# Kernel tuning notes

Measured on AMD Instinct MI355X. Metric: run time of the kernel, lower is better.

Reference implementation:

```python
import jax, jax.numpy as jnp
import numpy as np

BN_EPS = 1e-5


def grid_sample_bilinear(img, grid):
    """Torch F.grid_sample, mode=bilinear, padding_mode=zeros, align_corners=False.
    img: (B, C, H, W); grid: (B, N, 2) in [-1, 1] -> (B, C, N)."""
    B, C, H, W = img.shape
    x = ((grid[..., 0] + 1.0) * W - 1.0) * 0.5  # (B, N) pixel coords
    y = ((grid[..., 1] + 1.0) * H - 1.0) * 0.5
    x0 = jnp.floor(x)
    y0 = jnp.floor(y)
    x1 = x0 + 1.0
    y1 = y0 + 1.0
    wx1 = x - x0
    wx0 = 1.0 - wx1
    wy1 = y - y0
    wy0 = 1.0 - wy1
    img_flat = img.reshape(B, C, H * W)

    def corner(xi, yi, w):
        valid = (xi >= 0) & (xi <= W - 1) & (yi >= 0) & (yi <= H - 1)
        xi_c = jnp.clip(xi, 0, W - 1).astype(jnp.int32)
        yi_c = jnp.clip(yi, 0, H - 1).astype(jnp.int32)
        idx = yi_c * W + xi_c  # (B, N)
        vals = jnp.take_along_axis(img_flat, idx[:, None, :], axis=2)  # (B, C, N)
        return vals * (w * valid.astype(img.dtype))[:, None, :]

    return (corner(x0, y0, wx0 * wy0) + corner(x1, y0, wx1 * wy0)
            + corner(x0, y1, wx0 * wy1) + corner(x1, y1, wx1 * wy1))


def conv1x1(x, w, b):
    # x: (B, Cin, N), w: (Cout, Cin), b: (Cout,)
    return jnp.einsum('oi,bin->bon', w, x) + b[None, :, None]


def batchnorm1d_train(x, gamma, beta):
    # training-mode BN over (batch, length) per channel, biased variance
    mean = jnp.mean(x, axis=(0, 2), keepdims=True)
    var = jnp.mean((x - mean) ** 2, axis=(0, 2), keepdims=True)
    xn = (x - mean) * jax.lax.rsqrt(var + BN_EPS)
    return xn * gamma[None, :, None] + beta[None, :, None]


def setup_inputs() -> dict:
    key = jax.random.key(0)
    ks = jax.random.split(key, 12)
    B, N, CI, CP, H, W, R = 4, 16384, 256, 256, 64, 160, 4
    Cin = CI + CP
    Cb = CP // R

    def glorot(k, shape):
        fan_in = shape[1]
        return jax.random.normal(k, shape, dtype=jnp.float32) * (1.0 / np.sqrt(fan_in))

    return {
        'pts_img': jax.random.uniform(ks[0], (B, N, 2), dtype=jnp.float32, minval=-1.0, maxval=1.0),
        'img_feats': jax.random.normal(ks[1], (B, CI, H, W), dtype=jnp.float32),
        'pts_feats': jax.random.normal(ks[2], (B, CP, N), dtype=jnp.float32),
        'fusion_w': glorot(ks[3], (CP, Cin)),
        'fusion_b': jax.random.normal(ks[4], (CP,), dtype=jnp.float32) * 0.01,
        'bn_gamma': jnp.ones((CP,), dtype=jnp.float32),
        'bn_beta': jnp.zeros((CP,), dtype=jnp.float32),
        'ca1_w': glorot(ks[5], (Cb, CP)),
        'ca1_b': jax.random.normal(ks[6], (Cb,), dtype=jnp.float32) * 0.01,
        'ca2_w': glorot(ks[7], (CP, Cb)),
        'ca2_b': jax.random.normal(ks[8], (CP,), dtype=jnp.float32) * 0.01,
        'sa_w': glorot(ks[9], (Cb, CP)),
        'sa_b': jax.random.normal(ks[10], (Cb,), dtype=jnp.float32) * 0.01,
    }


def reference(pts_img, img_feats, pts_feats, fusion_w, fusion_b, bn_gamma, bn_beta,
              ca1_w, ca1_b, ca2_w, ca2_b, sa_w, sa_b):
    # grid_sample gather: (B, C_I, N)
    pts_wise_img_feats = grid_sample_bilinear(img_feats, pts_img)
    fusion = jnp.concatenate([pts_wise_img_feats, pts_feats], axis=1)  # (B, C_I+C_P, N)
    # fusion MLP: conv1x1 + BN + ReLU
    fusion = jax.nn.relu(batchnorm1d_train(conv1x1(fusion, fusion_w, fusion_b), bn_gamma, bn_beta))
    # spatial attention: max over channels of bottleneck conv, sigmoid gate
    spatial = jax.nn.sigmoid(jnp.max(conv1x1(fusion, sa_w, sa_b), axis=1, keepdims=True))
    fusion = spatial * fusion
    # channel attention: bottleneck MLP, global max-pool over points, sigmoid gate
    ca = conv1x1(jax.nn.relu(conv1x1(fusion, ca1_w, ca1_b)), ca2_w, ca2_b)  # (B, C_P, N)
    channel = jax.nn.sigmoid(jnp.max(ca, axis=2, keepdims=True))  # (B, C_P, 1)
    return channel * fusion
```

## Files before the change

kernel.cpp:

```cpp
#include <hip/hip_runtime.h>
#include <stdint.h>


typedef __attribute__((ext_vector_type(8))) short bf16x8;
typedef __attribute__((ext_vector_type(4))) float f32x4;

#define B_ 4
#define N_ 16384
#define H_ 64
#define W_ 160
#define HW_ (H_ * W_)
#define K_ 512

__device__ __forceinline__ float bf2f(unsigned short u) {
    union { unsigned int i; float f; } c; c.i = ((unsigned int)u) << 16; return c.f;
}
__device__ __forceinline__ unsigned short f2bf(float f) {
    union { float f; unsigned int i; } c; c.f = f;
    unsigned int u = c.i;
    return (unsigned short)((u + 0x7FFFu + ((u >> 16) & 1u)) >> 16);
}
__device__ __forceinline__ unsigned int fkey(float f) {
    union { float f; unsigned int u; int i; } c; c.f = f;
    return (c.i < 0) ? ~c.u : (c.u | 0x80000000u);
}
__device__ __forceinline__ float funkey(unsigned int k) {
    union { unsigned int u; float f; } c;
    c.u = (k & 0x80000000u) ? (k & 0x7FFFFFFFu) : ~k;
    return c.f;
}

__device__ __forceinline__ void async_copy16(void* lds, const void* g) {
#if defined(__has_builtin) && __has_builtin(__builtin_amdgcn_global_load_lds)
    __builtin_amdgcn_global_load_lds(
        (const __attribute__((address_space(1))) unsigned int*)g,
        (__attribute__((address_space(3))) unsigned int*)lds, 16, 0, 0);
#else
    *(uint4*)lds = *(const uint4*)g;
#endif
}

__global__ __launch_bounds__(256) void k_imgt(const float* __restrict__ img,
                                              unsigned short* __restrict__ imgT,
                                              const float* __restrict__ fw,
                                              const float* __restrict__ saw,
                                              const float* __restrict__ c1w,
                                              const float* __restrict__ c2w,
                                              unsigned short* WfB, unsigned short* saB,
                                              unsigned short* ca1B, unsigned short* ca2B,
                                              float* buckets, unsigned int* camax) {
    int t = threadIdx.x;
    int bx = blockIdx.x;
    if (bx < 2560) {
        __shared__ __align__(16) unsigned short tile[64 * 68];
        int hw0 = (bx % 160) * 64, c0 = ((bx / 160) & 3) * 64, b = bx / 640;
        const float* src = img + ((size_t)b * 256 + c0) * HW_ + hw0;
        int sub = (t & 15) * 4, grp = t >> 4;
#pragma unroll
        for (int it = 0; it < 4; ++it) {
            int cl = grp + it * 16;
            float4 v = *(const float4*)(src + (size_t)cl * HW_ + sub);
            ushort4 o;
            o.x = f2bf(v.x); o.y = f2bf(v.y); o.z = f2bf(v.z); o.w = f2bf(v.w);
            *(ushort4*)(tile + cl * 68 + sub) = o;
        }
        __syncthreads();
        unsigned short* dst = imgT + ((size_t)b * HW_ + hw0) * 256 + c0;
#pragma unroll
        for (int it = 0; it < 4; ++it) {
            int hwl = grp + it * 16;
            ushort4 o;
            o.x = tile[(sub + 0) * 68 + hwl];
            o.y = tile[(sub + 1) * 68 + hwl];
            o.z = tile[(sub + 2) * 68 + hwl];
            o.w = tile[(sub + 3) * 68 + hwl];
            *(ushort4*)(dst + (size_t)hwl * 256 + sub) = o;
        }
    } else {
        int j = bx - 2560;
        if (j == 0) {
            for (int i = t; i < 16 * 512; i += 256) buckets[i] = 0.f;
            for (int i = t; i < 8 * 1024; i += 256) camax[i] = 0u;
        }
        int i = j * 256 + t;
        if (i < 131072) WfB[i] = f2bf(fw[i]);
        else if (i < 147456) saB[i - 131072] = f2bf(saw[i - 131072]);
        else if (i < 163840) ca1B[i - 147456] = f2bf(c1w[i - 147456]);
        else if (i < 180224) ca2B[i - 163840] = f2bf(c2w[i - 163840]);
    }
}

__global__ __launch_bounds__(256, 4) void k_gemm1f(const unsigned short* __restrict__ WfB,
                                                   const float* __restrict__ pim,
                                                   const unsigned short* __restrict__ imgT,
                                                   const float* __restrict__ pts,
                                                   const float* __restrict__ fb,
                                                   unsigned short* __restrict__ Y,
                                                   float* __restrict__ buckets) {
    __shared__ __align__(16) char smem[38912];
    unsigned short* At = (unsigned short*)smem;
    unsigned short* Bt = (unsigned short*)(smem + 16384);
    unsigned short* tile = (unsigned short*)smem;
    uint4*  offs4 = (uint4*)(smem + 33792);
    float4* wts4  = (float4*)(smem + 34816);
    float* biasS = (float*)(smem + 35840);
    float* redS  = (float*)(smem + 36864);
    float* redQ  = (float*)(smem + 37888);

    int t = threadIdx.x;
    int n0 = blockIdx.x * 64, bb = blockIdx.y;
    int w = t >> 6, lane = t & 63, quad = lane >> 4, l15 = lane & 15;
    const unsigned short* imb = imgT + (size_t)bb * HW_ * 256;

    if (t < 64) {
        float2 g2 = *(const float2*)(pim + (size_t)((size_t)bb * N_ + n0 + t) * 2);
        float x = (g2.x + 1.0f) * (0.5f * W_) - 0.5f;
        float y = (g2.y + 1.0f) * (0.5f * H_) - 0.5f;
        float xf = floorf(x), yf = floorf(y);
        float wx1 = x - xf, wx0 = 1.0f - wx1;
        float wy1 = y - yf, wy0 = 1.0f - wy1;
        int x0 = (int)xf, y0 = (int)yf;
        int x1 = x0 + 1, y1 = y0 + 1;
        float vx0 = (x0 >= 0 && x0 < W_) ? 1.f : 0.f;
        float vx1 = (x1 >= 0 && x1 < W_) ? 1.f : 0.f;
        float vy0 = (y0 >= 0 && y0 < H_) ? 1.f : 0.f;
        float vy1 = (y1 >= 0 && y1 < H_) ? 1.f : 0.f;
        int cx0 = min(max(x0, 0), W_ - 1), cx1 = min(max(x1, 0), W_ - 1);
        int cy0 = min(max(y0, 0), H_ - 1), cy1 = min(max(y1, 0), H_ - 1);
        uint4 o4;
        o4.x = (unsigned)(cy0 * W_ + cx0);
        o4.y = (unsigned)(cy0 * W_ + cx1);
        o4.z = (unsigned)(cy1 * W_ + cx0);
        o4.w = (unsigned)(cy1 * W_ + cx1);
        offs4[t] = o4;
        float4 w4;
        w4.x = wx0 * wy0 * vx0 * vy0;
        w4.y = wx1 * wy0 * vx1 * vy0;
        w4.z = wx0 * wy1 * vx0 * vy1;
        w4.w = wx1 * wy1 * vx1 * vy1;
        wts4[t] = w4;
    }
    biasS[t] = fb[t];

    const f32x4 fzero = {0.f, 0.f, 0.f, 0.f};
    f32x4 acc[4][4];
#pragma unroll
    for (int i = 0; i < 4; ++i)
#pragma unroll
        for (int j = 0; j < 4; ++j) acc[i][j] = fzero;

    for (int kt = 0; kt < 16; ++kt) {
        int k0 = kt * 32;
        __syncthreads();
#pragma unroll
        for (int q = 0; q < 4; ++q) {
            int row = q * 64 + (t >> 2);
            async_copy16(At + (size_t)q * 2048 + (size_t)t * 8,
                         WfB + (size_t)row * K_ + k0 + (t & 3) * 8);
        }
        if (kt < 8) {
            int pt = t >> 2, cg = t & 3;
            uint4 o4 = offs4[pt];
            float4 w4 = wts4[pt];
            int ch = k0 + cg * 8;
            uint4 cA = *(const uint4*)(imb + (size_t)o4.x * 256 + ch);
            uint4 cB = *(const uint4*)(imb + (size_t)o4.y * 256 + ch);
            uint4 cC = *(const uint4*)(imb + (size_t)o4.z * 256 + ch);
            uint4 cD = *(const uint4*)(imb + (size_t)o4.w * 256 + ch);
            const unsigned short* pa = (const unsigned short*)&cA;
            const unsigned short* pb = (const unsigned short*)&cB;
            const unsigned short* pc = (const unsigned short*)&cC;
            const unsigned short* pd = (const unsigned short*)&cD;
            uint4 ov;
            unsigned short* po = (unsigned short*)&ov;
#pragma unroll
            for (int e = 0; e < 8; ++e)
                po[e] = f2bf(w4.x * bf2f(pa[e]) + w4.y * bf2f(pb[e]) +
                             w4.z * bf2f(pc[e]) + w4.w * bf2f(pd[e]));
            *(uint4*)(Bt + pt * 40 + cg * 8) = ov;
        } else {
            int c_local = t & 31, g = t >> 5;
            int c = (kt - 8) * 32 + c_local;
            const float* src = pts + ((size_t)bb * 256 + c) * (size_t)N_ + n0 + g * 8;
            float4 v0 = *(const float4*)(src + 0);
            float4 v1 = *(const float4*)(src + 4);
            unsigned short* dst = Bt + (size_t)(g * 8) * 40 + c_local;
            dst[0 * 40] = f2bf(v0.x); dst[1 * 40] = f2bf(v0.y);
            dst[2 * 40] = f2bf(v0.z); dst[3 * 40] = f2bf(v0.w);
            dst[4 * 40] = f2bf(v1.x); dst[5 * 40] = f2bf(v1.y);
            dst[6 * 40] = f2bf(v1.z); dst[7 * 40] = f2bf(v1.w);
        }
        __syncthreads();
        bf16x8 af[4], bv[4];
#pragma unroll
        for (int j = 0; j < 4; ++j)
            bv[j] = *(const bf16x8*)(Bt + (j * 16 + l15) * 40 + quad * 8);
#pragma unroll
        for (int i = 0; i < 4; ++i)
            af[i] = *(const bf16x8*)(At + (w * 64 + i * 16 + l15) * 32 + quad * 8);
#pragma unroll
        for (int i = 0; i < 4; ++i)
#pragma unroll
            for (int j = 0; j < 4; ++j)
                acc[i][j] = __builtin_amdgcn_mfma_f32_16x16x32_bf16(af[i], bv[j], acc[i][j], 0, 0, 0);
    }

    __syncthreads();
#pragma unroll
    for (int i = 0; i < 4; ++i) {
        int mloc = w * 64 + i * 16 + quad * 4;
        float b0 = biasS[mloc + 0], b1 = biasS[mloc + 1];
        float b2 = biasS[mloc + 2], b3 = biasS[mloc + 3];
        float s0 = 0.f, q0 = 0.f, s1 = 0.f, q1 = 0.f;
        float s2 = 0.f, q2 = 0.f, s3 = 0.f, q3 = 0.f;
#pragma unroll
        for (int j = 0; j < 4; ++j) {
            int n = j * 16 + l15;
            float y0 = acc[i][j][0] + b0;
            float y1 = acc[i][j][1] + b1;
            float y2 = acc[i][j][2] + b2;
            float y3 = acc[i][j][3] + b3;
            s0 += y0; q0 += y0 * y0;
            s1 += y1; q1 += y1 * y1;
            s2 += y2; q2 += y2 * y2;
            s3 += y3; q3 += y3 * y3;
            ushort4 o;
            o.x = f2bf(y0); o.y = f2bf(y1); o.z = f2bf(y2); o.w = f2bf(y3);
            *(ushort4*)(tile + n * 264 + mloc) = o;
        }
#pragma unroll
        for (int d = 1; d < 16; d <<= 1) {
            s0 += __shfl_xor(s0, d, 64); q0 += __shfl_xor(q0, d, 64);
            s1 += __shfl_xor(s1, d, 64); q1 += __shfl_xor(q1, d, 64);
            s2 += __shfl_xor(s2, d, 64); q2 += __shfl_xor(q2, d, 64);
            s3 += __shfl_xor(s3, d, 64); q3 += __shfl_xor(q3, d, 64);
        }
        if (l15 == 0) {
            redS[mloc + 0] = s0; redQ[mloc + 0] = q0;
            redS[mloc + 1] = s1; redQ[mloc + 1] = q1;
            redS[mloc + 2] = s2; redQ[mloc + 2] = q2;
            redS[mloc + 3] = s3; redQ[mloc + 3] = q3;
        }
    }
    __syncthreads();
    {
        float* bk = buckets + (size_t)(blockIdx.x & 15) * 512;
        atomicAdd(bk + t, redS[t]);
        atomicAdd(bk + 256 + t, redQ[t]);
    }
    size_t Yrow0 = ((size_t)bb * N_ + n0) * 256;
#pragma unroll
    for (int pass = 0; pass < 8; ++pass) {
        int row = pass * 8 + (t >> 5);
        int col = (t & 31) * 8;
        *(uint4*)(Y + Yrow0 + (size_t)row * 256 + col) = *(const uint4*)(tile + row * 264 + col);
    }
}

__global__ __launch_bounds__(256, 2) void k_gate(const unsigned short* __restrict__ Y,
                                                 const float* __restrict__ buckets,
                                                 const float* __restrict__ gamma,
                                                 const float* __restrict__ beta,
                                                 const unsigned short* __restrict__ saB,
                                                 const float* __restrict__ sab,
                                                 const unsigned short* __restrict__ c1B,
                                                 const float* __restrict__ c1b,
                                                 const unsigned short* __restrict__ c2B,
                                                 unsigned int* __restrict__ camax,
                                                 float* __restrict__ sp_g,
                                                 float* __restrict__ ss_out) {
    __shared__ __align__(16) unsigned short Ft[64 * 264];
    __shared__ __align__(16) unsigned short Ht[64 * 72];
    __shared__ float scS[256], shS[256];
    __shared__ float saPart[4][64];
    __shared__ float spL[64];
    int t = threadIdx.x;
    size_t pts0 = (size_t)blockIdx.x * 64;
    int b = (int)(pts0 >> 14);
    int w = t >> 6, lane = t & 63, quad = lane >> 4, l15 = lane & 15;
    int jrow = w * 16 + l15;

    bf16x8 bvs[8], bvc[8];
#pragma unroll
    for (int kt = 0; kt < 8; ++kt) {
        bvs[kt] = *(const bf16x8*)(saB + (size_t)jrow * 256 + kt * 32 + quad * 8);
        bvc[kt] = *(const bf16x8*)(c1B + (size_t)jrow * 256 + kt * 32 + quad * 8);
    }
    float sbias = sab[jrow];
    float cbias = c1b[jrow];

    {
        float s = 0.f, q = 0.f;
#pragma unroll
        for (int bk = 0; bk < 16; ++bk) {
            s += buckets[bk * 512 + t];
            q += buckets[bk * 512 + 256 + t];
        }
        const float inv = 1.0f / (float)(B_ * N_);
        float mean = s * inv;
        float var = q * inv - mean * mean;
        float sc = gamma[t] * rsqrtf(var + 1e-5f);
        float sh = beta[t] - mean * sc;
        scS[t] = sc;
        shS[t] = sh;
        if (blockIdx.x == 0) { ss_out[t] = sc; ss_out[256 + t] = sh; }
    }
    __syncthreads();

    int cc = (t * 8) & 255;
    float scr[8], shr[8];
#pragma unroll
    for (int e = 0; e < 8; ++e) { scr[e] = scS[cc + e]; shr[e] = shS[cc + e]; }
    for (int idx = t * 8; idx < 64 * 256; idx += 2048) {
        int r = idx >> 8;
        uint4 v = *(const uint4*)(Y + (pts0 + r) * 256 + cc);
        unsigned short* us = (unsigned short*)&v;
#pragma unroll
        for (int e = 0; e < 8; ++e) {
            float f = bf2f(us[e]) * scr[e] + shr[e];
            us[e] = f2bf(fmaxf(f, 0.f));
        }
        *(uint4*)(Ft + r * 264 + cc) = v;
    }
    __syncthreads();

    const f32x4 fzero = {0.f, 0.f, 0.f, 0.f};
    f32x4 accS[4], accC[4];
#pragma unroll
    for (int i = 0; i < 4; ++i) { accS[i] = fzero; accC[i] = fzero; }
#pragma unroll
    for (int kt = 0; kt < 8; ++kt) {
        bf16x8 af[4];
#pragma unroll
        for (int i = 0; i < 4; ++i)
            af[i] = *(const bf16x8*)(Ft + (i * 16 + l15) * 264 + kt * 32 + quad * 8);
#pragma unroll
        for (int i = 0; i < 4; ++i) {
            accS[i] = __builtin_amdgcn_mfma_f32_16x16x32_bf16(af[i], bvs[kt], accS[i], 0, 0, 0);
            accC[i] = __builtin_amdgcn_mfma_f32_16x16x32_bf16(af[i], bvc[kt], accC[i], 0, 0, 0);
        }
    }
#pragma unroll
    for (int i = 0; i < 4; ++i) {
#pragma unroll
        for (int r = 0; r < 4; ++r) {
            float v = accS[i][r] + sbias;
#pragma unroll
            for (int d = 1; d < 16; d <<= 1) v = fmaxf(v, __shfl_xor(v, d, 64));
            if (l15 == 0) saPart[w][i * 16 + quad * 4 + r] = v;
        }
    }
    __syncthreads();
    if (t < 64) {
        float m4 = fmaxf(fmaxf(saPart[0][t], saPart[1][t]),
                         fmaxf(saPart[2][t], saPart[3][t]));
        float sv = 1.0f / (1.0f + __expf(-m4));
        spL[t] = sv;
        sp_g[pts0 + t] = sv;
    }
    __syncthreads();

#pragma unroll
    for (int i = 0; i < 4; ++i) {
#pragma unroll
        for (int r = 0; r < 4; ++r) {
            int pt = i * 16 + quad * 4 + r;
            float hv = fmaxf(accC[i][r] * spL[pt] + cbias, 0.f);
            Ht[pt * 72 + jrow] = f2bf(hv);
        }
    }
    __syncthreads();

    {
        bf16x8 b2a[4], b2b[4];
#pragma unroll
        for (int mt = 0; mt < 4; ++mt) {
            b2a[mt] = *(const bf16x8*)(c2B + (size_t)(w * 64 + mt * 16 + l15) * 64 + quad * 8);
            b2b[mt] = *(const bf16x8*)(c2B + (size_t)(w * 64 + mt * 16 + l15) * 64 + 32 + quad * 8);
        }
        float vmax[4] = {-3e38f, -3e38f, -3e38f, -3e38f};
#pragma unroll
        for (int i = 0; i < 4; ++i) {
            bf16x8 a0 = *(const bf16x8*)(Ht + (i * 16 + l15) * 72 + quad * 8);
            bf16x8 a1 = *(const bf16x8*)(Ht + (i * 16 + l15) * 72 + 32 + quad * 8);
#pragma unroll
            for (int mt = 0; mt < 4; ++mt) {
                f32x4 acc = __builtin_amdgcn_mfma_f32_16x16x32_bf16(a0, b2a[mt], fzero, 0, 0, 0);
                acc = __builtin_amdgcn_mfma_f32_16x16x32_bf16(a1, b2b[mt], acc, 0, 0, 0);
#pragma unroll
                for (int r = 0; r < 4; ++r) vmax[mt] = fmaxf(vmax[mt], acc[r]);
            }
        }
        unsigned int* cam = camax + (size_t)(blockIdx.x & 7) * 1024 + b * 256;
#pragma unroll
        for (int mt = 0; mt < 4; ++mt) {
            float v = vmax[mt];
            v = fmaxf(v, __shfl_xor(v, 16, 64));
            v = fmaxf(v, __shfl_xor(v, 32, 64));
            if (quad == 0) atomicMax(cam + w * 64 + mt * 16 + l15, fkey(v));
        }
    }
}

__global__ __launch_bounds__(256) void k_out(const unsigned short* __restrict__ Y,
                                             const unsigned int* __restrict__ camax,
                                             const float* __restrict__ c2b,
                                             const float* __restrict__ ss,
                                             const float* __restrict__ sp_g,
                                             float* __restrict__ out) {
    __shared__ __align__(16) unsigned short tile[64 * 68];
    __shared__ float ch[64], scT[64], shT[64], spT[64];
    int t = threadIdx.x;
    int n0 = blockIdx.x * 64, m0 = blockIdx.y * 64, b = blockIdx.z;
    if (t < 64) {
        int m = m0 + t;
        unsigned int k = 0u;
#pragma unroll
        for (int bk = 0; bk < 8; ++bk) k = max(k, camax[bk * 1024 + b * 256 + m]);
        ch[t] = 1.0f / (1.0f + __expf(-(funkey(k) + c2b[m])));
        scT[t] = ss[m];
        shT[t] = ss[256 + m];
        spT[t] = sp_g[(size_t)b * N_ + n0 + t];
    }
    int sub = (t & 15) * 4, grp = t >> 4;
    const unsigned short* src = Y + ((size_t)b * N_ + n0) * 256 + m0;
#pragma unroll
    for (int it = 0; it < 4; ++it) {
        int nl = grp + it * 16;
        ushort4 v = *(const ushort4*)(src + (size_t)nl * 256 + sub);
        *(ushort4*)(tile + nl * 68 + sub) = v;
    }
    __syncthreads();
    float* dst = out + ((size_t)b * 256 + m0) * N_ + n0;
#pragma unroll
    for (int it = 0; it < 4; ++it) {
        int ml = grp + it * 16;
        float g = ch[ml], scv = scT[ml], shv = shT[ml];
        float4 o;
        o.x = fmaxf(bf2f(tile[(sub + 0) * 68 + ml]) * scv + shv, 0.f) * spT[sub + 0] * g;
        o.y = fmaxf(bf2f(tile[(sub + 1) * 68 + ml]) * scv + shv, 0.f) * spT[sub + 1] * g;
        o.z = fmaxf(bf2f(tile[(sub + 2) * 68 + ml]) * scv + shv, 0.f) * spT[sub + 2] * g;
        o.w = fmaxf(bf2f(tile[(sub + 3) * 68 + ml]) * scv + shv, 0.f) * spT[sub + 3] * g;
        *(float4*)(dst + (size_t)ml * N_ + sub) = o;
    }
}

extern "C" void kernel_launch(void* const* d_in, const int* in_sizes, int n_in,
                              void* d_out, int out_size, void* d_ws, size_t ws_size,
                              hipStream_t stream) {
    (void)in_sizes; (void)n_in; (void)out_size; (void)ws_size;
    const float* pts_img = (const float*)d_in[0];
    const float* img     = (const float*)d_in[1];
    const float* pts     = (const float*)d_in[2];
    const float* fw      = (const float*)d_in[3];
    const float* fbias   = (const float*)d_in[4];
    const float* gamma   = (const float*)d_in[5];
    const float* beta    = (const float*)d_in[6];
    const float* c1w     = (const float*)d_in[7];
    const float* c1b     = (const float*)d_in[8];
    const float* c2w     = (const float*)d_in[9];
    const float* c2b     = (const float*)d_in[10];
    const float* saw     = (const float*)d_in[11];
    const float* sab     = (const float*)d_in[12];
    float* out = (float*)d_out;

    char* ws = (char*)d_ws;
    unsigned short* imgT = (unsigned short*)(ws);
    unsigned short* Y    = (unsigned short*)(ws + 20971520);
    unsigned short* WfB  = (unsigned short*)(ws + 54525952);
    unsigned short* saB  = (unsigned short*)(ws + 54788096);
    unsigned short* ca1B = (unsigned short*)(ws + 54820864);
    unsigned short* ca2B = (unsigned short*)(ws + 54853632);
    float* buckets       = (float*)(ws + 54886400);
    unsigned int* camax  = (unsigned int*)(ws + 54919168);
    float* sp_g          = (float*)(ws + 54951936);
    float* ss            = (float*)(ws + 55214080);

    k_imgt<<<3264, 256, 0, stream>>>(img, imgT, fw, saw, c1w, c2w,
                                     WfB, saB, ca1B, ca2B, buckets, camax);
    k_gemm1f<<<dim3(256, 4), 256, 0, stream>>>(WfB, pts_img, imgT, pts, fbias, Y, buckets);
    k_gate<<<1024, 256, 0, stream>>>(Y, buckets, gamma, beta, saB, sab, ca1B, c1b,
                                     ca2B, camax, sp_g, ss);
    k_out<<<dim3(256, 4, 4), 256, 0, stream>>>(Y, camax, c2b, ss, sp_g, out);
}
```

Before: 248.4 us.

## Software-prefetch next K-tile gather and point features into registers

The global loads for the bilinear image gather and the point-feature tile of step kt+1 are now issued right after the barrier, before the MFMA work of step kt. The tile is converted and stored to shared memory at the start of the next iteration, so global latency is meant to hide behind compute instead of sitting between the two barriers. Sample offsets and weights are read from shared memory once, after an added barrier. This raises register pressure (four uint4 plus two float4 stay live across the MFMA loop), which may reduce occupancy.

```diff
diff --git a/kernel.cpp b/kernel.cpp
--- a/kernel.cpp
+++ b/kernel.cpp
@@ -141,6 +141,25 @@
         wts4[t] = w4;
     }
     biasS[t] = fb[t];
+    __syncthreads();
+
+    int pt = t >> 2, cg = t & 3;
+    float4 w4 = wts4[pt];
+    uint4 o4r = offs4[pt];
+    const unsigned short* pA = imb + (size_t)o4r.x * 256 + cg * 8;
+    const unsigned short* pB = imb + (size_t)o4r.y * 256 + cg * 8;
+    const unsigned short* pC = imb + (size_t)o4r.z * 256 + cg * 8;
+    const unsigned short* pD = imb + (size_t)o4r.w * 256 + cg * 8;
+    int c_local = t & 31, g = t >> 5;
+    const float* psrc = pts + ((size_t)bb * 256 + c_local) * (size_t)N_ + n0 + g * 8;
+
+    uint4 gA, gB, gC, gD;
+    float4 p0, p1;
+
+    gA = *(const uint4*)(pA);
+    gB = *(const uint4*)(pB);
+    gC = *(const uint4*)(pC);
+    gD = *(const uint4*)(pD);
 
     const f32x4 fzero = {0.f, 0.f, 0.f, 0.f};
     f32x4 acc[4][4];
@@ -152,45 +171,43 @@
     for (int kt = 0; kt < 16; ++kt) {
         int k0 = kt * 32;
         __syncthreads();
+        if (kt < 8) {
+            const unsigned short* qa = (const unsigned short*)&gA;
+            const unsigned short* qb = (const unsigned short*)&gB;
+            const unsigned short* qc = (const unsigned short*)&gC;
+            const unsigned short* qd = (const unsigned short*)&gD;
+            uint4 ov;
+            unsigned short* po = (unsigned short*)&ov;
+#pragma unroll
+            for (int e = 0; e < 8; ++e)
+                po[e] = f2bf(w4.x * bf2f(qa[e]) + w4.y * bf2f(qb[e]) +
+                             w4.z * bf2f(qc[e]) + w4.w * bf2f(qd[e]));
+            *(uint4*)(Bt + pt * 40 + cg * 8) = ov;
+        } else {
+            unsigned short* dst = Bt + (size_t)(g * 8) * 40 + c_local;
+            dst[0 * 40] = f2bf(p0.x); dst[1 * 40] = f2bf(p0.y);
+            dst[2 * 40] = f2bf(p0.z); dst[3 * 40] = f2bf(p0.w);
+            dst[4 * 40] = f2bf(p1.x); dst[5 * 40] = f2bf(p1.y);
+            dst[6 * 40] = f2bf(p1.z); dst[7 * 40] = f2bf(p1.w);
+        }
 #pragma unroll
         for (int q = 0; q < 4; ++q) {
             int row = q * 64 + (t >> 2);
             async_copy16(At + (size_t)q * 2048 + (size_t)t * 8,
                          WfB + (size_t)row * K_ + k0 + (t & 3) * 8);
         }
-        if (kt < 8) {
-            int pt = t >> 2, cg = t & 3;
-            uint4 o4 = offs4[pt];
-            float4 w4 = wts4[pt];
-            int ch = k0 + cg * 8;
-            uint4 cA = *(const uint4*)(imb + (size_t)o4.x * 256 + ch);
-            uint4 cB = *(const uint4*)(imb + (size_t)o4.y * 256 + ch);
-            uint4 cC = *(const uint4*)(imb + (size_t)o4.z * 256 + ch);
-            uint4 cD = *(const uint4*)(imb + (size_t)o4.w * 256 + ch);
-            const unsigned short* pa = (const unsigned short*)&cA;
-            const unsigned short* pb = (const unsigned short*)&cB;
-            const unsigned short* pc = (const unsigned short*)&cC;
-            const unsigned short* pd = (const unsigned short*)&cD;
-            uint4 ov;
-            unsigned short* po = (unsigned short*)&ov;
-#pragma unroll
-            for (int e = 0; e < 8; ++e)
-                po[e] = f2bf(w4.x * bf2f(pa[e]) + w4.y * bf2f(pb[e]) +
-                             w4.z * bf2f(pc[e]) + w4.w * bf2f(pd[e]));
-            *(uint4*)(Bt + pt * 40 + cg * 8) = ov;
-        } else {
-            int c_local = t & 31, g = t >> 5;
-            int c = (kt - 8) * 32 + c_local;
-            const float* src = pts + ((size_t)bb * 256 + c) * (size_t)N_ + n0 + g * 8;
-            float4 v0 = *(const float4*)(src + 0);
-            float4 v1 = *(const float4*)(src + 4);
-            unsigned short* dst = Bt + (size_t)(g * 8) * 40 + c_local;
-            dst[0 * 40] = f2bf(v0.x); dst[1 * 40] = f2bf(v0.y);
-            dst[2 * 40] = f2bf(v0.z); dst[3 * 40] = f2bf(v0.w);
-            dst[4 * 40] = f2bf(v1.x); dst[5 * 40] = f2bf(v1.y);
-            dst[6 * 40] = f2bf(v1.z); dst[7 * 40] = f2bf(v1.w);
-        }
         __syncthreads();
+        if (kt + 1 < 8) {
+            int ch = (kt + 1) * 32;
+            gA = *(const uint4*)(pA + ch);
+            gB = *(const uint4*)(pB + ch);
+            gC = *(const uint4*)(pC + ch);
+            gD = *(const uint4*)(pD + ch);
+        } else if (kt + 1 < 16) {
+            const float* s2 = psrc + (size_t)(kt + 1 - 8) * 32 * N_;
+            p0 = *(const float4*)(s2 + 0);
+            p1 = *(const float4*)(s2 + 4);
+        }
         bf16x8 af[4], bv[4];
 #pragma unroll
         for (int j = 0; j < 4; ++j)
```

Result: slower. 265.9 us (+7.0%).

## Prefetch gathered image tile and double-buffer weight and point loads in fused GEMM1

Applied to the files above, without the earlier changes.

The fused grid-sample plus GEMM kernel now gathers all 256 image channels for its 64 points into shared memory once, before the K loop. It double-buffers the weight tiles with async copies issued one step ahead, and register-prefetches point features two steps ahead. This removes one barrier per iteration and overlaps global loads with MFMA work. In exchange, shared memory roughly doubles and launch bounds drop to 2 blocks per CU, which lowers occupancy and may expose latency elsewhere.

```diff
diff --git a/kernel.cpp b/kernel.cpp
--- a/kernel.cpp
+++ b/kernel.cpp
@@ -90,22 +90,19 @@
     }
 }
 
-__global__ __launch_bounds__(256, 4) void k_gemm1f(const unsigned short* __restrict__ WfB,
+__global__ __launch_bounds__(256, 2) void k_gemm1f(const unsigned short* __restrict__ WfB,
                                                    const float* __restrict__ pim,
                                                    const unsigned short* __restrict__ imgT,
                                                    const float* __restrict__ pts,
                                                    const float* __restrict__ fb,
                                                    unsigned short* __restrict__ Y,
                                                    float* __restrict__ buckets) {
-    __shared__ __align__(16) char smem[38912];
-    unsigned short* At = (unsigned short*)smem;
-    unsigned short* Bt = (unsigned short*)(smem + 16384);
-    unsigned short* tile = (unsigned short*)smem;
-    uint4*  offs4 = (uint4*)(smem + 33792);
-    float4* wts4  = (float4*)(smem + 34816);
-    float* biasS = (float*)(smem + 35840);
-    float* redS  = (float*)(smem + 36864);
-    float* redQ  = (float*)(smem + 37888);
+    __shared__ __align__(16) char smem[75776];
+    unsigned short* Bimg = (unsigned short*)smem;
+    unsigned short* At   = (unsigned short*)(smem + 33792);
+    unsigned short* Btp  = (unsigned short*)(smem + 66560);
+    uint4*  offs4 = (uint4*)(smem + 66560);
+    float4* wts4  = (float4*)(smem + 66560 + 1024);
 
     int t = threadIdx.x;
     int n0 = blockIdx.x * 64, bb = blockIdx.y;
@@ -140,7 +137,47 @@
         w4.w = wx1 * wy1 * vx1 * vy1;
         wts4[t] = w4;
     }
-    biasS[t] = fb[t];
+    __syncthreads();
+
+#pragma unroll
+    for (int q = 0; q < 4; ++q) {
+        int row = q * 64 + (t >> 2);
+        async_copy16(At + (size_t)q * 2048 + (size_t)t * 8,
+                     WfB + (size_t)row * K_ + (t & 3) * 8);
+    }
+    {
+        int pt = t >> 2, cg = t & 3;
+        uint4 o4 = offs4[pt];
+        float4 w4 = wts4[pt];
+        const unsigned short* pA = imb + (size_t)o4.x * 256;
+        const unsigned short* pB = imb + (size_t)o4.y * 256;
+        const unsigned short* pC = imb + (size_t)o4.z * 256;
+        const unsigned short* pD = imb + (size_t)o4.w * 256;
+        unsigned short* brow = Bimg + pt * 264;
+#pragma unroll
+        for (int s = 0; s < 8; ++s) {
+            int ch = cg * 8 + s * 32;
+            uint4 cA = *(const uint4*)(pA + ch);
+            uint4 cB = *(const uint4*)(pB + ch);
+            uint4 cC = *(const uint4*)(pC + ch);
+            uint4 cD = *(const uint4*)(pD + ch);
+            const unsigned short* qa = (const unsigned short*)&cA;
+            const unsigned short* qb = (const unsigned short*)&cB;
+            const unsigned short* qc = (const unsigned short*)&cC;
+            const unsigned short* qd = (const unsigned short*)&cD;
+            uint4 ov;
+            unsigned short* po = (unsigned short*)&ov;
+#pragma unroll
+            for (int e = 0; e < 8; ++e)
+                po[e] = f2bf(w4.x * bf2f(qa[e]) + w4.y * bf2f(qb[e]) +
+                             w4.z * bf2f(qc[e]) + w4.w * bf2f(qd[e]));
+            *(uint4*)(brow + ch) = ov;
+        }
+    }
+
+    int c_local = t & 31, g = t >> 5;
+    const float* psrc = pts + ((size_t)bb * 256 + c_local) * (size_t)N_ + n0 + g * 8;
+    float4 pE0, pE1, pO0, pO1;
 
     const f32x4 fzero = {0.f, 0.f, 0.f, 0.f};
     f32x4 acc[4][4];
@@ -149,55 +186,44 @@
 #pragma unroll
         for (int j = 0; j < 4; ++j) acc[i][j] = fzero;
 
+#pragma unroll
     for (int kt = 0; kt < 16; ++kt) {
-        int k0 = kt * 32;
+        if (kt >= 8) {
+            float4 q0 = (kt & 1) ? pO0 : pE0;
+            float4 q1 = (kt & 1) ? pO1 : pE1;
+            unsigned short* dst = Btp + (kt & 1) * 2304 + (g * 8) * 36 + c_local;
+            dst[0 * 36] = f2bf(q0.x); dst[1 * 36] = f2bf(q0.y);
+            dst[2 * 36] = f2bf(q0.z); dst[3 * 36] = f2bf(q0.w);
+            dst[4 * 36] = f2bf(q1.x); dst[5 * 36] = f2bf(q1.y);
+            dst[6 * 36] = f2bf(q1.z); dst[7 * 36] = f2bf(q1.w);
+        }
+        if (kt >= 6 && kt < 14) {
+            const float* s2 = psrc + (size_t)(kt - 6) * 32 * N_;
+            float4 a0 = *(const float4*)(s2 + 0);
+            float4 a1 = *(const float4*)(s2 + 4);
+            if (kt & 1) { pO0 = a0; pO1 = a1; } else { pE0 = a0; pE1 = a1; }
+        }
         __syncthreads();
-#pragma unroll
-        for (int q = 0; q < 4; ++q) {
-            int row = q * 64 + (t >> 2);
-            async_copy16(At + (size_t)q * 2048 + (size_t)t * 8,
-                         WfB + (size_t)row * K_ + k0 + (t & 3) * 8);
-        }
-        if (kt < 8) {
-            int pt = t >> 2, cg = t & 3;
-            uint4 o4 = offs4[pt];
-            float4 w4 = wts4[pt];
-            int ch = k0 + cg * 8;
-            uint4 cA = *(const uint4*)(imb + (size_t)o4.x * 256 + ch);
-            uint4 cB = *(const uint4*)(imb + (size_t)o4.y * 256 + ch);
-            uint4 cC = *(const uint4*)(imb + (size_t)o4.z * 256 + ch);
-            uint4 cD = *(const uint4*)(imb + (size_t)o4.w * 256 + ch);
-            const unsigned short* pa = (const unsigned short*)&cA;
-            const unsigned short* pb = (const unsigned short*)&cB;
-            const unsigned short* pc = (const unsigned short*)&cC;
-            const unsigned short* pd = (const unsigned short*)&cD;
-            uint4 ov;
-            unsigned short* po = (unsigned short*)&ov;
-#pragma unroll
-            for (int e = 0; e < 8; ++e)
-                po[e] = f2bf(w4.x * bf2f(pa[e]) + w4.y * bf2f(pb[e]) +
-                             w4.z * bf2f(pc[e]) + w4.w * bf2f(pd[e]));
-            *(uint4*)(Bt + pt * 40 + cg * 8) = ov;
-        } else {
-            int c_local = t & 31, g = t >> 5;
-            int c = (kt - 8) * 32 + c_local;
-            const float* src = pts + ((size_t)bb * 256 + c) * (size_t)N_ + n0 + g * 8;
-            float4 v0 = *(const float4*)(src + 0);
-            float4 v1 = *(const float4*)(src + 4);
-            unsigned short* dst = Bt + (size_t)(g * 8) * 40 + c_local;
-            dst[0 * 40] = f2bf(v0.x); dst[1 * 40] = f2bf(v0.y);
-            dst[2 * 40] = f2bf(v0.z); dst[3 * 40] = f2bf(v0.w);
-            dst[4 * 40] = f2bf(v1.x); dst[5 * 40] = f2bf(v1.y);
-            dst[6 * 40] = f2bf(v1.z); dst[7 * 40] = f2bf(v1.w);
-        }
-        __syncthreads();
+        if (kt < 15) {
+            int k0n = (kt + 1) * 32;
+#pragma unroll
+            for (int q = 0; q < 4; ++q) {
+                int row = q * 64 + (t >> 2);
+                async_copy16(At + ((kt + 1) & 1) * 8192 + (size_t)q * 2048 + (size_t)t * 8,
+                             WfB + (size_t)row * K_ + k0n + (t & 3) * 8);
+            }
+        }
         bf16x8 af[4], bv[4];
 #pragma unroll
-        for (int j = 0; j < 4; ++j)
-            bv[j] = *(const bf16x8*)(Bt + (j * 16 + l15) * 40 + quad * 8);
+        for (int j = 0; j < 4; ++j) {
+            if (kt < 8)
+                bv[j] = *(const bf16x8*)(Bimg + (j * 16 + l15) * 264 + kt * 32 + quad * 8);
+            else
+                bv[j] = *(const bf16x8*)(Btp + (kt & 1) * 2304 + (j * 16 + l15) * 36 + quad * 8);
+        }
 #pragma unroll
         for (int i = 0; i < 4; ++i)
-            af[i] = *(const bf16x8*)(At + (w * 64 + i * 16 + l15) * 32 + quad * 8);
+            af[i] = *(const bf16x8*)(At + (kt & 1) * 8192 + (w * 64 + i * 16 + l15) * 32 + quad * 8);
 #pragma unroll
         for (int i = 0; i < 4; ++i)
 #pragma unroll
@@ -206,11 +232,17 @@
     }
 
     __syncthreads();
+    unsigned short* tile = (unsigned short*)smem;
+    float* biasF = (float*)(smem + 33792);
+    float* redS  = (float*)(smem + 33792 + 1024);
+    float* redQ  = (float*)(smem + 33792 + 2048);
+    biasF[t] = fb[t];
+    __syncthreads();
 #pragma unroll
     for (int i = 0; i < 4; ++i) {
         int mloc = w * 64 + i * 16 + quad * 4;
-        float b0 = biasS[mloc + 0], b1 = biasS[mloc + 1];
-        float b2 = biasS[mloc + 2], b3 = biasS[mloc + 3];
+        float b0 = biasF[mloc + 0], b1 = biasF[mloc + 1];
+        float b2 = biasF[mloc + 2], b3 = biasF[mloc + 3];
         float s0 = 0.f, q0 = 0.f, s1 = 0.f, q1 = 0.f;
         float s2 = 0.f, q2 = 0.f, s3 = 0.f, q3 = 0.f;
 #pragma unroll
```

After: 254.0 us. 1.02x slower.
